# Kernel tuning notes

Hardware: AMD Instinct MI355X
Metric: run time of the kernel (lower is better)

Reference implementation:

```python
import jax, jax.numpy as jnp
import numpy as np

B, N, E = 2, 32768, 32768
DIM = 3
MP_STEPS = 2
H = 32  # hidden width; original bug: depth == hidden width (range(hidden))


def _ln(x, g, b):
    m = jnp.mean(x, axis=-1, keepdims=True)
    v = jnp.var(x, axis=-1, keepdims=True)
    return (x - m) * jax.lax.rsqrt(v + 1e-5) * g + b


def _mlp(x, Win, bin_, Wh, bh, Wout, bout, lng=None, lnb=None):
    # Linear -> ReLU -> [LN] -> H x (Linear -> ReLU -> [LN]) -> Linear -> ReLU
    h = jax.nn.relu(x @ Win + bin_)
    if lng is not None:
        h = _ln(h, lng[0], lnb[0])
        def body(h, p):
            W, b_, g_, bb = p
            return _ln(jax.nn.relu(h @ W + b_), g_, bb), None
        h, _ = jax.lax.scan(body, h, (Wh, bh, lng[1:], lnb[1:]))
    else:
        def body(h, p):
            W, b_ = p
            return jax.nn.relu(h @ W + b_), None
        h, _ = jax.lax.scan(body, h, (Wh, bh))
    return jax.nn.relu(h @ Wout + bout)


def _mk(key, din, h, dout, ln, pref):
    ks = jax.random.split(key, 3)
    d = {
        pref + 'Win': jax.random.normal(ks[0], (din, h), jnp.float32) / np.sqrt(din).astype(np.float32),
        pref + 'bin': jnp.zeros((h,), jnp.float32),
        pref + 'Wh': jax.random.normal(ks[1], (h, h, h), jnp.float32) / np.sqrt(h).astype(np.float32),
        pref + 'bh': jnp.zeros((h, h), jnp.float32),
        pref + 'Wout': jax.random.normal(ks[2], (h, dout), jnp.float32) / np.sqrt(h).astype(np.float32),
        pref + 'bout': jnp.zeros((dout,), jnp.float32),
    }
    if ln:
        d[pref + 'lng'] = jnp.ones((h + 1, h), jnp.float32)
        d[pref + 'lnb'] = jnp.zeros((h + 1, h), jnp.float32)
    return d


def setup_inputs() -> dict:
    key = jax.random.key(0)
    ks = jax.random.split(key, 10)
    inp = {
        'nodes': jax.random.normal(ks[0], (B, N, 6), jnp.float32),
        'edges': jax.random.normal(ks[1], (B, E, 1), jnp.float32),
        'gvec': jax.random.normal(ks[2], (B,), jnp.float32),
        'senders': jax.random.randint(ks[3], (B, E), 0, N, jnp.int32),
        'receivers': jax.random.randint(ks[4], (B, E), 0, N, jnp.int32),
    }
    inp.update(_mk(ks[5], 6 + 1, H, 16, False, 'ne_'))          # node encoder: node_dim+global
    inp.update(_mk(ks[6], 1 + DIM + 1, H, 16, False, 'ed_'))    # edge encoder: edge_dim+dim+1
    inp.update(_mk(ks[7], 16 + 2 * 16 + 1, H, 16, True, 'pe_')) # edge processor
    inp.update(_mk(ks[8], 16 + 16 + 1, H, 16, True, 'pv_'))     # node processor
    inp.update(_mk(ks[9], 16, H, DIM, False, 'de_'))            # decoder
    return inp


def reference(nodes, edges, gvec, senders, receivers,
              ne_Win, ne_bin, ne_Wh, ne_bh, ne_Wout, ne_bout,
              ed_Win, ed_bin, ed_Wh, ed_bh, ed_Wout, ed_bout,
              pe_Win, pe_bin, pe_Wh, pe_bh, pe_Wout, pe_bout, pe_lng, pe_lnb,
              pv_Win, pv_bin, pv_Wh, pv_bh, pv_Wout, pv_bout, pv_lng, pv_lnb,
              de_Win, de_bin, de_Wh, de_bh, de_Wout, de_bout):
    g_node = jnp.broadcast_to(gvec[:, None, None], (B, N, 1))  # global repeated per node
    g_edge = jnp.broadcast_to(gvec[:, None, None], (B, E, 1))  # global repeated per edge
    x = jnp.concatenate([nodes, g_node], axis=-1)  # [B,N,7]

    # relative edge features from sender/receiver positions (first DIM cols)
    pos = x[..., :DIM]
    si = senders[:, :, None]
    ri = receivers[:, :, None]
    rel = jnp.take_along_axis(pos, si, axis=1) - jnp.take_along_axis(pos, ri, axis=1)  # [B,E,3]
    nrm = jnp.linalg.norm(rel, axis=-1, keepdims=True)
    e_in = jnp.concatenate([edges, rel, nrm], axis=-1)  # [B,E,5]

    ve = _mlp(x, ne_Win, ne_bin, ne_Wh, ne_bh, ne_Wout, ne_bout)       # [B,N,16]
    ee = _mlp(e_in, ed_Win, ed_bin, ed_Wh, ed_bh, ed_Wout, ed_bout)    # [B,E,16]

    seg = jax.vmap(lambda e, r: jax.ops.segment_sum(e, r, num_segments=N))

    for _ in range(MP_STEPS):
        # phi_e: gather sender/receiver node states, concat, edge MLP
        vs = jnp.take_along_axis(ve, si, axis=1)  # [B,E,16]
        vr = jnp.take_along_axis(ve, ri, axis=1)
        ee = _mlp(jnp.concatenate([ee, vs, vr, g_edge], axis=-1),
                  pe_Win, pe_bin, pe_Wh, pe_bh, pe_Wout, pe_bout, pe_lng, pe_lnb)
        # phi_v: scatter-add edge states into receiver nodes, concat, node MLP
        agg = seg(ee, receivers)  # [B,N,16]
        ve = _mlp(jnp.concatenate([agg, ve, g_node], axis=-1),
                  pv_Win, pv_bin, pv_Wh, pv_bh, pv_Wout, pv_bout, pv_lng, pv_lnb)

    return _mlp(ve, de_Win, de_bin, de_Wh, de_bh, de_Wout, de_bout)  # [B,N,3]
```

## Files before the change

### kernel.cpp

```cpp
#include <hip/hip_runtime.h>

#define BB 2
#define NN 32768
#define EN 32768

typedef unsigned int u32;
typedef __attribute__((ext_vector_type(8)))  short bf16x8;
typedef __attribute__((ext_vector_type(2)))  float f32x2;
typedef __attribute__((ext_vector_type(16))) float f32x16;

union U4 { uint4 u; bf16x8 h; };

__device__ __forceinline__ u32 pk2(float lo, float hi) {
    u32 r;
    asm("v_cvt_pk_bf16_f32 %0, %1, %2" : "=v"(r) : "v"(lo), "v"(hi));
    return r;
}

__device__ __forceinline__ float xor32_sum(float x) {
    float y = x;
    asm("v_permlane32_swap_b32 %0, %1" : "+v"(x), "+v"(y));
    return x + y;
}

// ... 15 lines not shown
        f32x2 sv = ((p0+p1)+(p2+p3)) + ((p4+p5)+(p6+p7));
        f32x2 ta = __builtin_elementwise_fma(p0,p0,
                   __builtin_elementwise_fma(p1,p1,
                   __builtin_elementwise_fma(p2,p2, p3*p3)));
        f32x2 tb = __builtin_elementwise_fma(p4,p4,
                   __builtin_elementwise_fma(p5,p5,
                   __builtin_elementwise_fma(p6,p6, p7*p7)));
        f32x2 tv = ta + tb;
        float s = xor32_sum(sv.x + sv.y);
        float t = xor32_sum(tv.x + tv.y);
        float mu  = s * (1.f/32.f);
        float var = fmaf(-mu, mu, t * (1.f/32.f));
        float rs  = rsqrtf(var + 1e-5f);
        float nt  = -mu * rs;
        f32x2 rs2 = {rs, rs}, nt2 = {nt, nt};
        p0 = __builtin_elementwise_fma(p0, rs2, nt2);
        p1 = __builtin_elementwise_fma(p1, rs2, nt2);
        p2 = __builtin_elementwise_fma(p2, rs2, nt2);
        p3 = __builtin_elementwise_fma(p3, rs2, nt2);
        p4 = __builtin_elementwise_fma(p4, rs2, nt2);
        p5 = __builtin_elementwise_fma(p5, rs2, nt2);
        p6 = __builtin_elementwise_fma(p6, rs2, nt2);
        p7 = __builtin_elementwise_fma(p7, rs2, nt2);
    }
    U4 c;
    c.u.x = pk2(p0.x,p0.y); c.u.y = pk2(p1.x,p1.y);
    c.u.z = pk2(p2.x,p2.y); c.u.w = pk2(p3.x,p3.y);
    B0 = c.h;
    c.u.x = pk2(p4.x,p4.y); c.u.y = pk2(p5.x,p5.y);
    c.u.z = pk2(p6.x,p6.y); c.u.w = pk2(p7.x,p7.y);
    B1 = c.h;
}

__device__ __forceinline__ f32x16 load_biasC(const float* WB, int base, int h) {
    const float4* p = (const float4*)(WB + base + h*16);
    float4 a = p[0], b = p[1], c = p[2], d = p[3];
    f32x16 C = {a.x,a.y,a.z,a.w, b.x,b.y,b.z,b.w,
                c.x,c.y,c.z,c.w, d.x,d.y,d.z,d.w};
    return C;
}

template<int NT, bool LN>
__device__ __forceinline__ f32x16 mlp32(const bf16x8* bIn,
    const u32* WL, const float* WB, int lane, int h)
{
    constexpr int HB = NT*256;
    constexpr int BO = HB + 16384;
    U4 c;
    f32x16 D = load_biasC(WB, 0, h);
    #pragma unroll
    for (int t = 0; t < NT; ++t) {
        c.u = *(const uint4*)(WL + t*256 + lane*4);
        D = MF32(c.h, bIn[t], D);
    }
    c.u = *(const uint4*)(WL + HB + lane*4);        bf16x8 w0 = c.h;
    c.u = *(const uint4*)(WL + HB + 256 + lane*4);  bf16x8 w1 = c.h;
    c.u = *(const uint4*)(WL + HB + 512 + lane*4);  bf16x8 x0 = c.h;
    c.u = *(const uint4*)(WL + HB + 768 + lane*4);  bf16x8 x1 = c.h;
    f32x16 pb = load_biasC(WB, 32, h);
    bf16x8 B0, B1;
    transform32<LN>(D, B0, B1);
    #pragma unroll 4
    for (int l = 0; l < 32; ++l) {
        const int lp = (l+2 < 32) ? l+2 : 31;
        c.u = *(const uint4*)(WL + HB + lp*512 + lane*4);       bf16x8 nw0 = c.h;
        c.u = *(const uint4*)(WL + HB + lp*512 + 256 + lane*4); bf16x8 nw1 = c.h;
        const int lb_ = (l+1 < 32) ? l+1 : 31;
        f32x16 nb = load_biasC(WB, 32 + lb_*32, h);
        f32x16 E = MF32(w0, B0, pb);
        E = MF32(w1, B1, E);
        transform32<LN>(E, B0, B1);
        w0 = x0; w1 = x1; x0 = nw0; x1 = nw1; pb = nb;
    }
    c.u = *(const uint4*)(WL + BO + lane*4);        bf16x8 o0 = c.h;
    c.u = *(const uint4*)(WL + BO + 256 + lane*4);  bf16x8 o1 = c.h;
    f32x16 Co = load_biasC(WB, 1056, h);
    f32x16 O = MF32(o0, B0, Co);
    O = MF32(o1, B1, O);
    return O;
}

__device__ __forceinline__ void stage_weights32(
    u32* WL, float* WB, const u32* __restrict__ Wp,
    const float* __restrict__ bin, const float* __restrict__ bhid,
    const float* __restrict__ bo, int wtot, int nbo, int tid, int nthr)
{
    const int lane  = tid & 63;
    const int base0 = (tid >> 6) * 256;
    const int step  = (nthr >> 6) * 256;
    for (int C = base0; C < wtot; C += step)
        __builtin_amdgcn_global_load_lds(
            (const __attribute__((address_space(1))) u32*)(Wp + C + lane*4),
            (__attribute__((address_space(3))) u32*)(WL + C), 16, 0, 0);
    for (int i = tid; i < 1088; i += nthr) {
        float v;
        if (i < 32) {
            int w = i, hh = w>>4, r = w&15;
            int f = (r&3) + 8*(r>>2) + 4*hh;
            v = bin[f];
        } else if (i < 1056) {
            int l = (i-32)>>5, w = (i-32)&31, hh = w>>4, r = w&15;
            int f = (r&3) + 8*(r>>2) + 4*hh;
            v = bhid[l*32 + f];
        } else {
            int w = i-1056, hh = w>>4, r = w&15;
            int f = (r&3) + 8*(r>>2) + 4*hh;
            v = (f < nbo) ? bo[f] : 0.f;
        }
        WB[i] = v;
    }
    __syncthreads();
}

__device__ __forceinline__ void pack_body32(
    const float* __restrict__ Win, const float* __restrict__ Wh,
    const float* __restrict__ Wout, const float* __restrict__ lng,
    u32* __restrict__ dst, int din, int dout, int NT, int lb, int tid)
{
    int t = lb * 256 + tid;
    int binW = NT * 256;
    int tot = binW + 16384 + 512;
    if (t >= tot) return;
    float lo, hi;
    if (t < binW) {
        int tt = t>>8, rem = t&255, ln_ = rem>>2, d = rem&3;
        int hh = ln_>>5, m = ln_&31;
        int f0 = 16*tt + 4*hh + 2*(d&1) + 8*(d>>1);
        lo = (f0   < din) ? Win[f0*32 + m]     : 0.f;
        hi = (f0+1 < din) ? Win[(f0+1)*32 + m] : 0.f;
    } else if (t < binW + 16384) {
        int u = t - binW, l = u>>9, v = u&511;
        int tt = v>>8, rem = v&255, ln_ = rem>>2, d = rem&3;
        int hh = ln_>>5, m = ln_&31;
        int f0 = 16*tt + 4*hh + 2*(d&1) + 8*(d>>1);
        lo = Wh[l*1024 + f0*32 + m];
        hi = Wh[l*1024 + (f0+1)*32 + m];
        if (lng) { lo *= lng[l*32 + f0]; hi *= lng[l*32 + f0 + 1]; }
    } else {
        int u = t - binW - 16384;
        int tt = u>>8, rem = u&255, ln_ = rem>>2, d = rem&3;
        int hh = ln_>>5, m = ln_&31;
        int f0 = 16*tt + 4*hh + 2*(d&1) + 8*(d>>1);
        lo = (m < dout) ? Wout[f0*dout + m]     : 0.f;
        hi = (m < dout) ? Wout[(f0+1)*dout + m] : 0.f;
        if (lng) { lo *= lng[1024 + f0]; hi *= lng[1024 + f0 + 1]; }
    }
    dst[t] = pk2(lo, hi);
}

__device__ __forceinline__ void fold_body(
    const float* __restrict__ Wh,   const float* __restrict__ bh,
    const float* __restrict__ Wout, const float* __restrict__ bout,
    const float* __restrict__ lnb,  float* __restrict__ fb, int lb, int tid)
{
    int j = lb * 256 + tid;
    if (j < 1024) {
        int l = j >> 5, jj = j & 31;
        float acc = bh[j];
        #pragma unroll
        for (int k = 0; k < 32; ++k)
            acc = fmaf(lnb[l*32 + k], Wh[l*1024 + k*32 + jj], acc);
        fb[j] = acc;
    } else if (j < 1024 + 16) {
        int jj = j - 1024;
        float acc = bout[jj];
        #pragma unroll
        for (int k = 0; k < 32; ++k)
            acc = fmaf(lnb[1024 + k], Wout[k*16 + jj], acc);
        fb[j] = acc;
    }
}

__global__ __launch_bounds__(256) void prep_kernel(
    const float* ne_Win, const float* ne_Wh, const float* ne_Wout,
    const float* ed_Win, const float* ed_Wh, const float* ed_Wout,
    const float* pe_Win, const float* pe_Wh, const float* pe_Wout,
    const float* pe_lng, const float* pe_lnb, const float* pe_bh, const float* pe_bout,
    const float* pv_Win, const float* pv_Wh, const float* pv_Wout,
    const float* pv_lng, const float* pv_lnb, const float* pv_bh, const float* pv_bout,
    const float* de_Win, const float* de_Wh, const float* de_Wout,
    u32* Wne, u32* Wed, u32* Wpe, u32* Wpv, u32* Wde,
    float* Fpe, float* Fpv)
{
    int bx = blockIdx.x, tid = threadIdx.x;
    if      (bx < 67)  pack_body32(ne_Win, ne_Wh, ne_Wout, nullptr, Wne,  7, 16, 1, bx,       tid);
    else if (bx < 134) pack_body32(ed_Win, ed_Wh, ed_Wout, nullptr, Wed,  5, 16, 1, bx - 67,  tid);
    else if (bx < 204) pack_body32(pe_Win, pe_Wh, pe_Wout, pe_lng,  Wpe, 49, 16, 4, bx - 134, tid);
    else if (bx < 273) pack_body32(pv_Win, pv_Wh, pv_Wout, pv_lng,  Wpv, 33, 16, 3, bx - 204, tid);
    else if (bx < 340) pack_body32(de_Win, de_Wh, de_Wout, nullptr, Wde, 16,  3, 1, bx - 273, tid);
    else if (bx < 345) fold_body(pe_Wh, pe_bh, pe_Wout, pe_bout, pe_lnb, Fpe, bx - 340, tid);
    else               fold_body(pv_Wh, pv_bh, pv_Wout, pv_bout, pv_lnb, Fpv, bx - 345, tid);
}

__device__ __forceinline__ bf16x8 stage_chunk(const float* __restrict__ arr,
                                              size_t e, int h)
{
    const int off = h*4;
    float4 a = *(const float4*)(arr + e*16 + off);
    float4 b = *(const float4*)(arr + e*16 + off + 8);
    U4 c;
    c.u.x = pk2(a.x, a.y); c.u.y = pk2(a.z, a.w);
    c.u.z = pk2(b.x, b.y); c.u.w = pk2(b.z, b.w);
    return c.h;
}

#define WAVE_SETUP \
    const int lane = threadIdx.x & 63; \
    const int wid  = threadIdx.x >> 6; \
    const int el = lane & 31, h = lane >> 5;

__global__ __launch_bounds__(512, 4) void encode_kernel(
    const float* __restrict__ nodes, const float* __restrict__ edges,
    const float* __restrict__ gvec,
    const int* __restrict__ senders, const int* __restrict__ receivers,
    const u32* __restrict__ Wne, const float* __restrict__ ne_bin,
    const float* __restrict__ ne_bh, const float* __restrict__ ne_bout,
    const u32* __restrict__ Wed, const float* __restrict__ ed_bin,
    const float* __restrict__ ed_bh, const float* __restrict__ ed_bout,
    float* __restrict__ ve, float* __restrict__ ee)
{
    __shared__ __align__(16) u32 SL[17152 + 1088];
    u32* WL = SL;
    float* WB = (float*)(SL + 17152);
    WAVE_SETUP
    const bool edge_stage = blockIdx.x >= 256;
    stage_weights32(WL, WB,
                    edge_stage ? Wed : Wne,
                    edge_stage ? ed_bin : ne_bin,
                    edge_stage ? ed_bh : ne_bh,
                    edge_stage ? ed_bout : ne_bout,
                    17152, 16, threadIdx.x, 512);
    const int lb = edge_stage ? (blockIdx.x - 256) : blockIdx.x;
    const int e = (lb*8 + wid)*32 + el;
    const int b = e >> 15;
    bf16x8 a0;
    {
        uint4 w; w.x = 0u; w.y = 0u; w.z = 0u; w.w = 0u;
        if (!edge_stage) {
            if (h == 0) {
                float2 v01 = *(const float2*)(nodes + (size_t)e*6);
                float2 v23 = *(const float2*)(nodes + (size_t)e*6 + 2);
                w.x = pk2(v01.x, v01.y); w.y = pk2(v23.x, v23.y);
            } else {
                float2 v45 = *(const float2*)(nodes + (size_t)e*6 + 4);
                w.x = pk2(v45.x, v45.y); w.y = pk2(gvec[b], 0.f);
            }
        } else {
            int s = senders[e], r = receivers[e];
            const float* ps = nodes + ((size_t)b*NN + s)*6;
            const float* pr = nodes + ((size_t)b*NN + r)*6;
            float2 s01 = *(const float2*)ps; float s2v = ps[2];
            float2 r01 = *(const float2*)pr; float r2v = pr[2];
            float r0 = s01.x - r01.x, r1 = s01.y - r01.y, r2 = s2v - r2v;
            if (h == 0) {
                w.x = pk2(edges[e], r0); w.y = pk2(r1, r2);
            } else {
                w.x = pk2(sqrtf(r0*r0 + r1*r1 + r2*r2), 0.f);
            }
        }
        U4 c; c.u = w; a0 = c.h;
    }
    float* dst = edge_stage ? ee : ve;
    f32x16 O = mlp32<1, false>(&a0, WL, WB, lane, h);
    float4 s1, s2;
    s1.x = fmaxf(O[0], 0.f); s1.y = fmaxf(O[1], 0.f);
    s1.z = fmaxf(O[2], 0.f); s1.w = fmaxf(O[3], 0.f);
    s2.x = fmaxf(O[4], 0.f); s2.y = fmaxf(O[5], 0.f);
    s2.z = fmaxf(O[6], 0.f); s2.w = fmaxf(O[7], 0.f);
    *(float4*)(dst + (size_t)e*16 + h*4)     = s1;
    *(float4*)(dst + (size_t)e*16 + h*4 + 8) = s2;
}

__global__ __launch_bounds__(512, 2) void edge_update_kernel(
    const float* __restrict__ gvec,
    const int* __restrict__ senders, const int* __restrict__ receivers,
    const float* __restrict__ ve, float* __restrict__ ee, float* __restrict__ agg,
    const u32* __restrict__ Wp, const float* __restrict__ bin,
    const float* __restrict__ fb)
{
    __shared__ __align__(16) u32 SL[17920 + 1088 + 8*544];
    u32* WL = SL;
    float* WB = (float*)(SL + 17920);
    WAVE_SETUP
    float* X = (float*)(SL + 19008) + wid*544;
    stage_weights32(WL, WB, Wp, bin, fb, fb + 1024, 17920, 16, threadIdx.x, 512);
    const int e0 = (blockIdx.x*8 + wid)*32;
    const int e  = e0 + el;
    const int b  = e >> 15;
    const int s  = senders[e], r_ = receivers[e];
    bf16x8 a[4];
    a[0] = stage_chunk(ee, (size_t)e, h);
    a[1] = stage_chunk(ve, (size_t)b*NN + s, h);
    a[2] = stage_chunk(ve, (size_t)b*NN + r_, h);
    {
        uint4 w; w.x = (h == 0) ? pk2(gvec[b], 0.f) : 0u;
        w.y = 0u; w.z = 0u; w.w = 0u;
        U4 c; c.u = w; a[3] = c.h;
    }
    f32x16 O = mlp32<4, true>(a, WL, WB, lane, h);
    float4 s1, s2;
    s1.x = fmaxf(O[0], 0.f); s1.y = fmaxf(O[1], 0.f);
    s1.z = fmaxf(O[2], 0.f); s1.w = fmaxf(O[3], 0.f);
    s2.x = fmaxf(O[4], 0.f); s2.y = fmaxf(O[5], 0.f);
    s2.z = fmaxf(O[6], 0.f); s2.w = fmaxf(O[7], 0.f);
    *(float4*)(ee + (size_t)e*16 + h*4)     = s1;
    *(float4*)(ee + (size_t)e*16 + h*4 + 8) = s2;
    *(float4*)(X + el*17 + h*4)     = s1;
    *(float4*)(X + el*17 + h*4 + 8) = s2;
    const int feat = lane & 15;
    #pragma unroll
    for (int rr = 0; rr < 8; ++rr) {
        int m = (lane >> 4)*8 + rr;
        float v = X[m*17 + feat];
        int rc = __shfl(r_, m);
        int eg = e0 + m;
        atomicAdd(agg + ((size_t)(eg >> 15)*NN + rc)*16 + feat, v);
    }
}

template<bool DEC>
__global__ __launch_bounds__(512, 2) void node_update_kernel(
    const float* __restrict__ gvec,
    const float* __restrict__ agg, float* __restrict__ ve,
    const u32* __restrict__ Wp, const float* __restrict__ bin,
    const float* __restrict__ fb,
    const u32* __restrict__ Wde, const float* __restrict__ de_bin,
    const float* __restrict__ de_bh, const float* __restrict__ de_bout,
    float* __restrict__ out)
{
    __shared__ __align__(16) u32 SL[DEC ? (18752 + 17152 + 1088) : 18752];
    u32* WL = SL;
    float* WB = (float*)(SL + 17664);
    u32* WL2 = SL + 18752;
    float* WB2 = (float*)(SL + 18752 + 17152);
    WAVE_SETUP
    stage_weights32(WL, WB, Wp, bin, fb, fb + 1024, 17664, 16, threadIdx.x, 512);
    if (DEC)
        stage_weights32(WL2, WB2, Wde, de_bin, de_bh, de_bout, 17152, 3, threadIdx.x, 512);
    const int e = (blockIdx.x*8 + wid)*32 + el;
    const int b = e >> 15;
    bf16x8 a[3];
    a[0] = stage_chunk(agg, (size_t)e, h);
    a[1] = stage_chunk(ve,  (size_t)e, h);
    {
        uint4 w; w.x = (h == 0) ? pk2(gvec[b], 0.f) : 0u;
        w.y = 0u; w.z = 0u; w.w = 0u;
        U4 c; c.u = w; a[2] = c.h;
    }
    f32x16 O = mlp32<3, true>(a, WL, WB, lane, h);
    if (!DEC) {
        float4 s1, s2;
        s1.x = fmaxf(O[0], 0.f); s1.y = fmaxf(O[1], 0.f);
        s1.z = fmaxf(O[2], 0.f); s1.w = fmaxf(O[3], 0.f);
        s2.x = fmaxf(O[4], 0.f); s2.y = fmaxf(O[5], 0.f);
        s2.z = fmaxf(O[6], 0.f); s2.w = fmaxf(O[7], 0.f);
        *(float4*)(ve + (size_t)e*16 + h*4)     = s1;
        *(float4*)(ve + (size_t)e*16 + h*4 + 8) = s2;
    } else {
        bf16x8 D0, D1;
        transform32<false>(O, D0, D1);
        f32x16 O2 = mlp32<1, false>(&D0, WL2, WB2, lane, h);
        if (h == 0) {
            out[(size_t)e*3 + 0] = fmaxf(O2[0], 0.f);
            out[(size_t)e*3 + 1] = fmaxf(O2[1], 0.f);
            out[(size_t)e*3 + 2] = fmaxf(O2[2], 0.f);
        }
    }
}

extern "C" void kernel_launch(void* const* d_in, const int* in_sizes, int n_in,
                              void* d_out, int out_size, void* d_ws, size_t ws_size,
                              hipStream_t stream)
{
    const float* nodes     = (const float*)d_in[0];
    const float* edges     = (const float*)d_in[1];
    const float* gvec      = (const float*)d_in[2];
    const int*   senders   = (const int*)  d_in[3];
    const int*   receivers = (const int*)  d_in[4];

    const float* ne_Win  = (const float*)d_in[5];
    const float* ne_bin  = (const float*)d_in[6];
    const float* ne_Wh   = (const float*)d_in[7];
    const float* ne_bh   = (const float*)d_in[8];
    const float* ne_Wout = (const float*)d_in[9];
    const float* ne_bout = (const float*)d_in[10];

    const float* ed_Win  = (const float*)d_in[11];
    const float* ed_bin  = (const float*)d_in[12];
    const float* ed_Wh   = (const float*)d_in[13];
    const float* ed_bh   = (const float*)d_in[14];
    const float* ed_Wout = (const float*)d_in[15];
    const float* ed_bout = (const float*)d_in[16];

    const float* pe_Win  = (const float*)d_in[17];
    const float* pe_bin  = (const float*)d_in[18];
    const float* pe_Wh   = (const float*)d_in[19];
    const float* pe_bh   = (const float*)d_in[20];
    const float* pe_Wout = (const float*)d_in[21];
    const float* pe_bout = (const float*)d_in[22];
    const float* pe_lng  = (const float*)d_in[23];
    const float* pe_lnb  = (const float*)d_in[24];

    const float* pv_Win  = (const float*)d_in[25];
    const float* pv_bin  = (const float*)d_in[26];
    const float* pv_Wh   = (const float*)d_in[27];
    const float* pv_bh   = (const float*)d_in[28];
    const float* pv_Wout = (const float*)d_in[29];
    const float* pv_bout = (const float*)d_in[30];
    const float* pv_lng  = (const float*)d_in[31];
    const float* pv_lnb  = (const float*)d_in[32];

    const float* de_Win  = (const float*)d_in[33];
    const float* de_bin  = (const float*)d_in[34];
    const float* de_Wh   = (const float*)d_in[35];
    const float* de_bh   = (const float*)d_in[36];
    const float* de_Wout = (const float*)d_in[37];
    const float* de_bout = (const float*)d_in[38];

    float* ve   = (float*)d_ws;
    float* ee   = ve   + (size_t)1048576;
    float* agg0 = ee   + (size_t)1048576;
    float* agg1 = agg0 + (size_t)1048576;
    u32* Wne = (u32*)(agg1 + (size_t)1048576);
    u32* Wed = Wne + 17152;
    u32* Wpe = Wed + 17152;
    u32* Wpv = Wpe + 17920;
    u32* Wde = Wpv + 17664;
    float* Fpe = (float*)(Wde + 17152);
    float* Fpv = Fpe + 1040;

    prep_kernel<<<350, dim3(256), 0, stream>>>(
        ne_Win, ne_Wh, ne_Wout,
        ed_Win, ed_Wh, ed_Wout,
        pe_Win, pe_Wh, pe_Wout, pe_lng, pe_lnb, pe_bh, pe_bout,
        pv_Win, pv_Wh, pv_Wout, pv_lng, pv_lnb, pv_bh, pv_bout,
        de_Win, de_Wh, de_Wout,
        Wne, Wed, Wpe, Wpv, Wde, Fpe, Fpv);

    hipMemsetAsync(agg0, 0, (size_t)2 * 1048576 * sizeof(float), stream);

    encode_kernel<<<512, dim3(512), 0, stream>>>(nodes, edges, gvec, senders, receivers,
        Wne, ne_bin, ne_bh, ne_bout,
        Wed, ed_bin, ed_bh, ed_bout, ve, ee);

    edge_update_kernel<<<256, dim3(512), 0, stream>>>(gvec, senders, receivers,
        ve, ee, agg0, Wpe, pe_bin, Fpe);
    node_update_kernel<false><<<256, dim3(512), 0, stream>>>(gvec, agg0, ve,
        Wpv, pv_bin, Fpv, Wde, de_bin, de_bh, de_bout, (float*)d_out);
    edge_update_kernel<<<256, dim3(512), 0, stream>>>(gvec, senders, receivers,
        ve, ee, agg1, Wpe, pe_bin, Fpe);
    node_update_kernel<true><<<256, dim3(512), 0, stream>>>(gvec, agg1, ve,
        Wpv, pv_bin, Fpv, Wde, de_bin, de_bh, de_bout, (float*)d_out);
}
```

Before: 241.6 us.

## Fold LayerNorm mean subtraction into post-matmul affine correction for LN MLPs

Adds an mlp32_ln path in which each hidden layer multiplies the un-normalized ReLU output (bf16) by the gamma-folded weights. The LayerNorm is applied afterwards as rs*E + (-mu*rs)*rho + beta, where rho = column sums of the gamma-scaled weights, precomputed in prep_kernel. The intent is to take the per-layer normalize pass off the critical path before the next MFMA, so the statistics run in parallel with the matmul. The cost is a larger bias table in LDS (rho/beta per layer), extra prep blocks, and precision risk because raw activations are quantized to bf16 before normalization.

```diff
diff --git a/kernel.cpp b/kernel.cpp
--- a/kernel.cpp
+++ b/kernel.cpp
@@ -71,12 +71,28 @@
     B1 = c.h;
 }
 
+__device__ __forceinline__ void stats8(
+    f32x2 p0, f32x2 p1, f32x2 p2, f32x2 p3,
+    f32x2 p4, f32x2 p5, f32x2 p6, f32x2 p7, float& rs, float& q)
+{
+    f32x2 sv = ((p0+p1)+(p2+p3)) + ((p4+p5)+(p6+p7));
+    f32x2 ta = __builtin_elementwise_fma(p0,p0,
+               __builtin_elementwise_fma(p1,p1,
+               __builtin_elementwise_fma(p2,p2, p3*p3)));
+    f32x2 tb = __builtin_elementwise_fma(p4,p4,
+               __builtin_elementwise_fma(p5,p5,
+               __builtin_elementwise_fma(p6,p6, p7*p7)));
+    f32x2 tv = ta + tb;
+    float s = xor32_sum(sv.x + sv.y);
+    float t = xor32_sum(tv.x + tv.y);
+    float mu  = s * (1.f/32.f);
+    float var = fmaf(-mu, mu, t * (1.f/32.f));
+    rs = rsqrtf(var + 1e-5f);
+    q  = -mu * rs;
+}
+
 __device__ __forceinline__ f32x16 load_biasC(const float* WB, int base, int h) {
-    const float4* p = (const float4*)(WB + base + h*16);
-    float4 a = p[0], b = p[1], c = p[2], d = p[3];
-    f32x16 C = {a.x,a.y,a.z,a.w, b.x,b.y,b.z,b.w,
-                c.x,c.y,c.z,c.w, d.x,d.y,d.z,d.w};
-    return C;
+    return *(const f32x16*)(WB + base + h*16);
 }
 
 template<int NT, bool LN>
@@ -119,18 +135,131 @@
     return O;
 }
 
-__device__ __forceinline__ void stage_weights32(
-    u32* WL, float* WB, const u32* __restrict__ Wp,
-    const float* __restrict__ bin, const float* __restrict__ bhid,
-    const float* __restrict__ bo, int wtot, int nbo, int tid, int nthr)
-{
-    const int lane  = tid & 63;
-    const int base0 = (tid >> 6) * 256;
-    const int step  = (nthr >> 6) * 256;
-    for (int C = base0; C < wtot; C += step)
+#define LN_POST(E1, E2) \
+    { \
+        f32x2 q2 = {q, q}, rs2 = {rs, rs}; \
+        f32x2 b0 = {bet[0],bet[1]}, b1 = {bet[2],bet[3]}, b2 = {bet[4],bet[5]}, b3 = {bet[6],bet[7]}; \
+        f32x2 b4 = {bet[8],bet[9]}, b5 = {bet[10],bet[11]}, b6 = {bet[12],bet[13]}, b7 = {bet[14],bet[15]}; \
+        f32x2 r0 = {rho[0],rho[1]}, r1 = {rho[2],rho[3]}, r2 = {rho[4],rho[5]}, r3 = {rho[6],rho[7]}; \
+        f32x2 r4 = {rho[8],rho[9]}, r5 = {rho[10],rho[11]}, r6 = {rho[12],rho[13]}, r7 = {rho[14],rho[15]}; \
+        f32x2 c0 = __builtin_elementwise_fma(q2, r0, b0); \
+        f32x2 c1 = __builtin_elementwise_fma(q2, r1, b1); \
+        f32x2 c2 = __builtin_elementwise_fma(q2, r2, b2); \
+        f32x2 c3 = __builtin_elementwise_fma(q2, r3, b3); \
+        f32x2 c4 = __builtin_elementwise_fma(q2, r4, b4); \
+        f32x2 c5 = __builtin_elementwise_fma(q2, r5, b5); \
+        f32x2 c6 = __builtin_elementwise_fma(q2, r6, b6); \
+        f32x2 c7 = __builtin_elementwise_fma(q2, r7, b7); \
+        f32x2 e; \
+        e = (f32x2){E1[0],E1[1]};   c0 = __builtin_elementwise_fma(rs2, e, c0); \
+        e = (f32x2){E1[2],E1[3]};   c1 = __builtin_elementwise_fma(rs2, e, c1); \
+        e = (f32x2){E1[4],E1[5]};   c2 = __builtin_elementwise_fma(rs2, e, c2); \
+        e = (f32x2){E1[6],E1[7]};   c3 = __builtin_elementwise_fma(rs2, e, c3); \
+        e = (f32x2){E1[8],E1[9]};   c4 = __builtin_elementwise_fma(rs2, e, c4); \
+        e = (f32x2){E1[10],E1[11]}; c5 = __builtin_elementwise_fma(rs2, e, c5); \
+        e = (f32x2){E1[12],E1[13]}; c6 = __builtin_elementwise_fma(rs2, e, c6); \
+        e = (f32x2){E1[14],E1[15]}; c7 = __builtin_elementwise_fma(rs2, e, c7); \
+        e = (f32x2){E2[0],E2[1]};   p0 = __builtin_elementwise_fma(rs2, e, c0); \
+        e = (f32x2){E2[2],E2[3]};   p1 = __builtin_elementwise_fma(rs2, e, c1); \
+        e = (f32x2){E2[4],E2[5]};   p2 = __builtin_elementwise_fma(rs2, e, c2); \
+        e = (f32x2){E2[6],E2[7]};   p3 = __builtin_elementwise_fma(rs2, e, c3); \
+        e = (f32x2){E2[8],E2[9]};   p4 = __builtin_elementwise_fma(rs2, e, c4); \
+        e = (f32x2){E2[10],E2[11]}; p5 = __builtin_elementwise_fma(rs2, e, c5); \
+        e = (f32x2){E2[12],E2[13]}; p6 = __builtin_elementwise_fma(rs2, e, c6); \
+        e = (f32x2){E2[14],E2[15]}; p7 = __builtin_elementwise_fma(rs2, e, c7); \
+    }
+
+template<int NT>
+__device__ __forceinline__ f32x16 mlp32_ln(const bf16x8* bIn,
+    const u32* WL, const float* WB, int lane, int h)
+{
+    constexpr int HB = NT*256;
+    constexpr int BO = HB + 16384;
+    U4 c;
+    f32x16 Z;
+    #pragma unroll
+    for (int i = 0; i < 16; ++i) Z[i] = 0.f;
+    f32x16 D = load_biasC(WB, 0, h);
+    #pragma unroll
+    for (int t = 0; t < NT; ++t) {
+        c.u = *(const uint4*)(WL + t*256 + lane*4);
+        D = MF32(c.h, bIn[t], D);
+    }
+    const f32x2 zz = {0.f, 0.f};
+    f32x2 p0 = {D[0],D[1]},  p1 = {D[2],D[3]},  p2 = {D[4],D[5]},  p3 = {D[6],D[7]};
+    f32x2 p4 = {D[8],D[9]},  p5 = {D[10],D[11]},p6 = {D[12],D[13]},p7 = {D[14],D[15]};
+    p0 = __builtin_elementwise_max(p0, zz); p1 = __builtin_elementwise_max(p1, zz);
+    p2 = __builtin_elementwise_max(p2, zz); p3 = __builtin_elementwise_max(p3, zz);
+    p4 = __builtin_elementwise_max(p4, zz); p5 = __builtin_elementwise_max(p5, zz);
+    p6 = __builtin_elementwise_max(p6, zz); p7 = __builtin_elementwise_max(p7, zz);
+    float rs, q;
+    stats8(p0,p1,p2,p3,p4,p5,p6,p7, rs, q);
+    bf16x8 H0, H1;
+    {
+        U4 cc;
+        cc.u.x = pk2(p0.x,p0.y); cc.u.y = pk2(p1.x,p1.y);
+        cc.u.z = pk2(p2.x,p2.y); cc.u.w = pk2(p3.x,p3.y); H0 = cc.h;
+        cc.u.x = pk2(p4.x,p4.y); cc.u.y = pk2(p5.x,p5.y);
+        cc.u.z = pk2(p6.x,p6.y); cc.u.w = pk2(p7.x,p7.y); H1 = cc.h;
+    }
+    c.u = *(const uint4*)(WL + HB + lane*4);        bf16x8 w0 = c.h;
+    c.u = *(const uint4*)(WL + HB + 256 + lane*4);  bf16x8 w1 = c.h;
+    c.u = *(const uint4*)(WL + HB + 512 + lane*4);  bf16x8 x0 = c.h;
+    c.u = *(const uint4*)(WL + HB + 768 + lane*4);  bf16x8 x1 = c.h;
+    f32x16 bet = load_biasC(WB, 32, h);
+    f32x16 rho = load_biasC(WB, 64, h);
+    #pragma unroll 2
+    for (int l = 0; l < 32; ++l) {
+        f32x16 E1 = MF32(w0, H0, Z);
+        f32x16 E2 = MF32(w1, H1, Z);
+        const int lp = (l+2 < 32) ? l+2 : 31;
+        c.u = *(const uint4*)(WL + HB + lp*512 + lane*4);       bf16x8 nw0 = c.h;
+        c.u = *(const uint4*)(WL + HB + lp*512 + 256 + lane*4); bf16x8 nw1 = c.h;
+        const int lb_ = (l+1 < 32) ? l+1 : 31;
+        f32x16 betN = load_biasC(WB, 32 + lb_*64, h);
+        f32x16 rhoN = load_biasC(WB, 64 + lb_*64, h);
+        LN_POST(E1, E2)
+        p0 = __builtin_elementwise_max(p0, zz); p1 = __builtin_elementwise_max(p1, zz);
+        p2 = __builtin_elementwise_max(p2, zz); p3 = __builtin_elementwise_max(p3, zz);
+        p4 = __builtin_elementwise_max(p4, zz); p5 = __builtin_elementwise_max(p5, zz);
+        p6 = __builtin_elementwise_max(p6, zz); p7 = __builtin_elementwise_max(p7, zz);
+        stats8(p0,p1,p2,p3,p4,p5,p6,p7, rs, q);
+        {
+            U4 cc;
+            cc.u.x = pk2(p0.x,p0.y); cc.u.y = pk2(p1.x,p1.y);
+            cc.u.z = pk2(p2.x,p2.y); cc.u.w = pk2(p3.x,p3.y); H0 = cc.h;
+            cc.u.x = pk2(p4.x,p4.y); cc.u.y = pk2(p5.x,p5.y);
+            cc.u.z = pk2(p6.x,p6.y); cc.u.w = pk2(p7.x,p7.y); H1 = cc.h;
+        }
+        w0 = x0; w1 = x1; x0 = nw0; x1 = nw1; bet = betN; rho = rhoN;
+    }
+    c.u = *(const uint4*)(WL + BO + lane*4);        bf16x8 o0 = c.h;
+    c.u = *(const uint4*)(WL + BO + 256 + lane*4);  bf16x8 o1 = c.h;
+    bet = load_biasC(WB, 2080, h);
+    rho = load_biasC(WB, 2112, h);
+    f32x16 E1 = MF32(o0, H0, Z);
+    f32x16 E2 = MF32(o1, H1, Z);
+    LN_POST(E1, E2)
+    f32x16 O = {p0.x,p0.y, p1.x,p1.y, p2.x,p2.y, p3.x,p3.y,
+                p4.x,p4.y, p5.x,p5.y, p6.x,p6.y, p7.x,p7.y};
+    return O;
+}
+
+__device__ __forceinline__ void stage_dma(u32* WL, const u32* __restrict__ Wp,
+                                          int wtot, int tid, int nthr)
+{
+    const int lane = tid & 63;
+    const int step = (nthr >> 6) * 256;
+    for (int C = (tid >> 6)*256; C < wtot; C += step)
         __builtin_amdgcn_global_load_lds(
             (const __attribute__((address_space(1))) u32*)(Wp + C + lane*4),
             (__attribute__((address_space(3))) u32*)(WL + C), 16, 0, 0);
+}
+
+__device__ __forceinline__ void stage_bias(float* WB,
+    const float* __restrict__ bin, const float* __restrict__ bhid,
+    const float* __restrict__ bo, int nbo, int tid, int nthr)
+{
     for (int i = tid; i < 1088; i += nthr) {
         float v;
         if (i < 32) {
@@ -148,6 +277,46 @@
         }
         WB[i] = v;
     }
+}
+
+__device__ __forceinline__ void stage_bias_ln(float* WB,
+    const float* __restrict__ bin, const float* __restrict__ F,
+    int tid, int nthr)
+{
+    for (int i = tid; i < 2144; i += nthr) {
+        float v;
+        if (i < 32) {
+            int hh = i>>4, r = i&15;
+            int f = (r&3) + 8*(r>>2) + 4*hh;
+            v = bin[f];
+        } else {
+            int u = i - 32, l = u>>6, w = u&63, sel = w>>5, ww = w&31;
+            int hh = ww>>4, r = ww&15;
+            int f = (r&3) + 8*(r>>2) + 4*hh;
+            if (l < 32) v = sel ? F[1040 + l*32 + f] : F[l*32 + f];
+            else        v = (f < 16) ? (sel ? F[2064 + f] : F[1024 + f]) : 0.f;
+        }
+        WB[i] = v;
+    }
+}
+
+__device__ __forceinline__ void stage_weights32(
+    u32* WL, float* WB, const u32* __restrict__ Wp,
+    const float* __restrict__ bin, const float* __restrict__ bhid,
+    const float* __restrict__ bo, int wtot, int nbo, int tid, int nthr)
+{
+    stage_dma(WL, Wp, wtot, tid, nthr);
+    stage_bias(WB, bin, bhid, bo, nbo, tid, nthr);
+    __syncthreads();
+}
+
+__device__ __forceinline__ void stage_weights32_ln(
+    u32* WL, float* WB, const u32* __restrict__ Wp,
+    const float* __restrict__ bin, const float* __restrict__ F,
+    int wtot, int tid, int nthr)
+{
+    stage_dma(WL, Wp, wtot, tid, nthr);
+    stage_bias_ln(WB, bin, F, tid, nthr);
     __syncthreads();
 }
 
@@ -190,23 +359,23 @@
 __device__ __forceinline__ void fold_body(
     const float* __restrict__ Wh,   const float* __restrict__ bh,
     const float* __restrict__ Wout, const float* __restrict__ bout,
-    const float* __restrict__ lnb,  float* __restrict__ fb, int lb, int tid)
+    const float* __restrict__ vec,  float* __restrict__ dst, int lb, int tid)
 {
     int j = lb * 256 + tid;
     if (j < 1024) {
         int l = j >> 5, jj = j & 31;
-        float acc = bh[j];
+        float acc = bh ? bh[j] : 0.f;
         #pragma unroll
         for (int k = 0; k < 32; ++k)
-            acc = fmaf(lnb[l*32 + k], Wh[l*1024 + k*32 + jj], acc);
-        fb[j] = acc;
+            acc = fmaf(vec[l*32 + k], Wh[l*1024 + k*32 + jj], acc);
+        dst[j] = acc;
     } else if (j < 1024 + 16) {
         int jj = j - 1024;
-        float acc = bout[jj];
+        float acc = bout ? bout[jj] : 0.f;
         #pragma unroll
         for (int k = 0; k < 32; ++k)
-            acc = fmaf(lnb[1024 + k], Wout[k*16 + jj], acc);
-        fb[j] = acc;
+            acc = fmaf(vec[1024 + k], Wout[k*16 + jj], acc);
+        dst[j] = acc;
     }
 }
 
@@ -227,8 +396,10 @@
     else if (bx < 204) pack_body32(pe_Win, pe_Wh, pe_Wout, pe_lng,  Wpe, 49, 16, 4, bx - 134, tid);
     else if (bx < 273) pack_body32(pv_Win, pv_Wh, pv_Wout, pv_lng,  Wpv, 33, 16, 3, bx - 204, tid);
     else if (bx < 340) pack_body32(de_Win, de_Wh, de_Wout, nullptr, Wde, 16,  3, 1, bx - 273, tid);
-    else if (bx < 345) fold_body(pe_Wh, pe_bh, pe_Wout, pe_bout, pe_lnb, Fpe, bx - 340, tid);
-    else               fold_body(pv_Wh, pv_bh, pv_Wout, pv_bout, pv_lnb, Fpv, bx - 345, tid);
+    else if (bx < 345) fold_body(pe_Wh, pe_bh, pe_Wout, pe_bout, pe_lnb, Fpe,        bx - 340, tid);
+    else if (bx < 350) fold_body(pe_Wh, nullptr, pe_Wout, nullptr, pe_lng, Fpe+1040, bx - 345, tid);
+    else if (bx < 355) fold_body(pv_Wh, pv_bh, pv_Wout, pv_bout, pv_lnb, Fpv,        bx - 350, tid);
+    else               fold_body(pv_Wh, nullptr, pv_Wout, nullptr, pv_lng, Fpv+1040, bx - 355, tid);
 }
 
 __device__ __forceinline__ bf16x8 stage_chunk(const float* __restrict__ arr,
@@ -241,6 +412,18 @@
     c.u.x = pk2(a.x, a.y); c.u.y = pk2(a.z, a.w);
     c.u.z = pk2(b.x, b.y); c.u.w = pk2(b.z, b.w);
     return c.h;
+}
+
+__device__ __forceinline__ void store_relu(float* __restrict__ dst, size_t e,
+                                           int h, f32x16 O)
+{
+    float4 s1, s2;
+    s1.x = fmaxf(O[0], 0.f); s1.y = fmaxf(O[1], 0.f);
+    s1.z = fmaxf(O[2], 0.f); s1.w = fmaxf(O[3], 0.f);
+    s2.x = fmaxf(O[4], 0.f); s2.y = fmaxf(O[5], 0.f);
+    s2.z = fmaxf(O[6], 0.f); s2.w = fmaxf(O[7], 0.f);
+    *(float4*)(dst + e*16 + h*4)     = s1;
+    *(float4*)(dst + e*16 + h*4 + 8) = s2;
 }
 
 #define WAVE_SETUP \
@@ -258,7 +441,7 @@
     const float* __restrict__ ed_bh, const float* __restrict__ ed_bout,
     float* __restrict__ ve, float* __restrict__ ee)
 {
-    __shared__ __align__(16) u32 SL[17152 + 1088];
+    __shared__ __align__(64) u32 SL[17152 + 1088];
     u32* WL = SL;
     float* WB = (float*)(SL + 17152);
     WAVE_SETUP
@@ -301,13 +484,7 @@
     }
     float* dst = edge_stage ? ee : ve;
     f32x16 O = mlp32<1, false>(&a0, WL, WB, lane, h);
-    float4 s1, s2;
-    s1.x = fmaxf(O[0], 0.f); s1.y = fmaxf(O[1], 0.f);
-    s1.z = fmaxf(O[2], 0.f); s1.w = fmaxf(O[3], 0.f);
-    s2.x = fmaxf(O[4], 0.f); s2.y = fmaxf(O[5], 0.f);
-    s2.z = fmaxf(O[6], 0.f); s2.w = fmaxf(O[7], 0.f);
-    *(float4*)(dst + (size_t)e*16 + h*4)     = s1;
-    *(float4*)(dst + (size_t)e*16 + h*4 + 8) = s2;
+    store_relu(dst, (size_t)e, h, O);
 }
 
 __global__ __launch_bounds__(512, 2) void edge_update_kernel(
@@ -315,14 +492,14 @@
     const int* __restrict__ senders, const int* __restrict__ receivers,
     const float* __restrict__ ve, float* __restrict__ ee, float* __restrict__ agg,
     const u32* __restrict__ Wp, const float* __restrict__ bin,
-    const float* __restrict__ fb)
-{
-    __shared__ __align__(16) u32 SL[17920 + 1088 + 8*544];
+    const float* __restrict__ F)
+{
+    __shared__ __align__(64) u32 SL[17920 + 2144 + 8*544];
     u32* WL = SL;
     float* WB = (float*)(SL + 17920);
     WAVE_SETUP
-    float* X = (float*)(SL + 19008) + wid*544;
-    stage_weights32(WL, WB, Wp, bin, fb, fb + 1024, 17920, 16, threadIdx.x, 512);
+    float* X = (float*)(SL + 20064) + wid*544;
+    stage_weights32_ln(WL, WB, Wp, bin, F, 17920, threadIdx.x, 512);
     const int e0 = (blockIdx.x*8 + wid)*32;
     const int e  = e0 + el;
     const int b  = e >> 15;
@@ -336,7 +513,7 @@
         w.y = 0u; w.z = 0u; w.w = 0u;
         U4 c; c.u = w; a[3] = c.h;
     }
-    f32x16 O = mlp32<4, true>(a, WL, WB, lane, h);
+    f32x16 O = mlp32_ln<4>(a, WL, WB, lane, h);
     float4 s1, s2;
     s1.x = fmaxf(O[0], 0.f); s1.y = fmaxf(O[1], 0.f);
     s1.z = fmaxf(O[2], 0.f); s1.w = fmaxf(O[3], 0.f);
@@ -362,20 +539,21 @@
     const float* __restrict__ gvec,
     const float* __restrict__ agg, float* __restrict__ ve,
     const u32* __restrict__ Wp, const float* __restrict__ bin,
-    const float* __restrict__ fb,
+    const float* __restrict__ F,
     const u32* __restrict__ Wde, const float* __restrict__ de_bin,
     const float* __restrict__ de_bh, const float* __restrict__ de_bout,
     float* __restrict__ out)
 {
-    __shared__ __align__(16) u32 SL[DEC ? (18752 + 17152 + 1088) : 18752];
+    __shared__ __align__(64) u32 SL[DEC ? (19808 + 17152 + 1088) : 19808];
     u32* WL = SL;
     float* WB = (float*)(SL + 17664);
-    u32* WL2 = SL + 18752;
-    float* WB2 = (float*)(SL + 18752 + 17152);
+    u32* WL2 = SL + 19808;
+    float* WB2 = (float*)(SL + 19808 + 17152);
     WAVE_SETUP
-    stage_weights32(WL, WB, Wp, bin, fb, fb + 1024, 17664, 16, threadIdx.x, 512);
+    stage_weights32_ln(WL, WB, Wp, bin, F, 17664, threadIdx.x, 512);
     if (DEC)
-        stage_weights32(WL2, WB2, Wde, de_bin, de_bh, de_bout, 17152, 3, threadIdx.x, 512);
+        stage_weights32(WL2, WB2, Wde, de_bin, de_bh, de_bout, 17152, 3,
+                        threadIdx.x, 512);
     const int e = (blockIdx.x*8 + wid)*32 + el;
     const int b = e >> 15;
     bf16x8 a[3];
@@ -386,15 +564,9 @@
         w.y = 0u; w.z = 0u; w.w = 0u;
         U4 c; c.u = w; a[2] = c.h;
     }
-    f32x16 O = mlp32<3, true>(a, WL, WB, lane, h);
+    f32x16 O = mlp32_ln<3>(a, WL, WB, lane, h);
     if (!DEC) {
-        float4 s1, s2;
-        s1.x = fmaxf(O[0], 0.f); s1.y = fmaxf(O[1], 0.f);
-        s1.z = fmaxf(O[2], 0.f); s1.w = fmaxf(O[3], 0.f);
-        s2.x = fmaxf(O[4], 0.f); s2.y = fmaxf(O[5], 0.f);
-        s2.z = fmaxf(O[6], 0.f); s2.w = fmaxf(O[7], 0.f);
-        *(float4*)(ve + (size_t)e*16 + h*4)     = s1;
-        *(float4*)(ve + (size_t)e*16 + h*4 + 8) = s2;
+        store_relu(ve, (size_t)e, h, O);
     } else {
         bf16x8 D0, D1;
         transform32<false>(O, D0, D1);
@@ -466,9 +638,9 @@
     u32* Wpv = Wpe + 17920;
     u32* Wde = Wpv + 17664;
     float* Fpe = (float*)(Wde + 17152);
-    float* Fpv = Fpe + 1040;
-
-    prep_kernel<<<350, dim3(256), 0, stream>>>(
+    float* Fpv = Fpe + 2080;
+
+    prep_kernel<<<360, dim3(256), 0, stream>>>(
         ne_Win, ne_Wh, ne_Wout,
         ed_Win, ed_Wh, ed_Wout,
         pe_Win, pe_Wh, pe_Wout, pe_lng, pe_lnb, pe_bh, pe_bout,
```

New measurement: 244.1 us. No clear change (+1.1%).

## Store node/edge states as bf16 and fold global feature into per-batch input bias

Applied to the files above, without the earlier changes.

Intermediate node and edge states are now stored as packed bf16 instead of fp32, which halves gather/store traffic in the edge and node update kernels and removes the per-load fp32-to-bf16 conversion. The global-vector input column is folded into a per-batch input bias computed in prep_kernel, so the first-layer K tiles drop from 4 to 3 (edge) and from 3 to 2 (node). Blocks pick the bias by batch index, and the bias load becomes a single vector load. This adds bf16 rounding of the stored states and relies on the block-to-batch mapping (blockIdx & 128).

```diff
diff --git a/kernel.cpp b/kernel.cpp
--- a/kernel.cpp
+++ b/kernel.cpp
@@ -72,11 +72,7 @@
 }
 
 __device__ __forceinline__ f32x16 load_biasC(const float* WB, int base, int h) {
-    const float4* p = (const float4*)(WB + base + h*16);
-    float4 a = p[0], b = p[1], c = p[2], d = p[3];
-    f32x16 C = {a.x,a.y,a.z,a.w, b.x,b.y,b.z,b.w,
-                c.x,c.y,c.z,c.w, d.x,d.y,d.z,d.w};
-    return C;
+    return *(const f32x16*)(WB + base + h*16);
 }
 
 template<int NT, bool LN>
@@ -119,18 +115,21 @@
     return O;
 }
 
-__device__ __forceinline__ void stage_weights32(
-    u32* WL, float* WB, const u32* __restrict__ Wp,
-    const float* __restrict__ bin, const float* __restrict__ bhid,
-    const float* __restrict__ bo, int wtot, int nbo, int tid, int nthr)
-{
-    const int lane  = tid & 63;
-    const int base0 = (tid >> 6) * 256;
-    const int step  = (nthr >> 6) * 256;
-    for (int C = base0; C < wtot; C += step)
+__device__ __forceinline__ void stage_dma(u32* WL, const u32* __restrict__ Wp,
+                                          int wtot, int tid, int nthr)
+{
+    const int lane = tid & 63;
+    const int step = (nthr >> 6) * 256;
+    for (int C = (tid >> 6)*256; C < wtot; C += step)
         __builtin_amdgcn_global_load_lds(
             (const __attribute__((address_space(1))) u32*)(Wp + C + lane*4),
             (__attribute__((address_space(3))) u32*)(WL + C), 16, 0, 0);
+}
+
+__device__ __forceinline__ void stage_bias(float* WB,
+    const float* __restrict__ bin, const float* __restrict__ bhid,
+    const float* __restrict__ bo, int nbo, int tid, int nthr)
+{
     for (int i = tid; i < 1088; i += nthr) {
         float v;
         if (i < 32) {
@@ -148,6 +147,15 @@
         }
         WB[i] = v;
     }
+}
+
+__device__ __forceinline__ void stage_weights32(
+    u32* WL, float* WB, const u32* __restrict__ Wp,
+    const float* __restrict__ bin, const float* __restrict__ bhid,
+    const float* __restrict__ bo, int wtot, int nbo, int tid, int nthr)
+{
+    stage_dma(WL, Wp, wtot, tid, nthr);
+    stage_bias(WB, bin, bhid, bo, nbo, tid, nthr);
     __syncthreads();
 }
 
@@ -215,20 +223,32 @@
     const float* ed_Win, const float* ed_Wh, const float* ed_Wout,
     const float* pe_Win, const float* pe_Wh, const float* pe_Wout,
     const float* pe_lng, const float* pe_lnb, const float* pe_bh, const float* pe_bout,
+    const float* pe_bin,
     const float* pv_Win, const float* pv_Wh, const float* pv_Wout,
     const float* pv_lng, const float* pv_lnb, const float* pv_bh, const float* pv_bout,
+    const float* pv_bin,
     const float* de_Win, const float* de_Wh, const float* de_Wout,
+    const float* gvec,
     u32* Wne, u32* Wed, u32* Wpe, u32* Wpv, u32* Wde,
     float* Fpe, float* Fpv)
 {
     int bx = blockIdx.x, tid = threadIdx.x;
     if      (bx < 67)  pack_body32(ne_Win, ne_Wh, ne_Wout, nullptr, Wne,  7, 16, 1, bx,       tid);
     else if (bx < 134) pack_body32(ed_Win, ed_Wh, ed_Wout, nullptr, Wed,  5, 16, 1, bx - 67,  tid);
-    else if (bx < 204) pack_body32(pe_Win, pe_Wh, pe_Wout, pe_lng,  Wpe, 49, 16, 4, bx - 134, tid);
-    else if (bx < 273) pack_body32(pv_Win, pv_Wh, pv_Wout, pv_lng,  Wpv, 33, 16, 3, bx - 204, tid);
-    else if (bx < 340) pack_body32(de_Win, de_Wh, de_Wout, nullptr, Wde, 16,  3, 1, bx - 273, tid);
-    else if (bx < 345) fold_body(pe_Wh, pe_bh, pe_Wout, pe_bout, pe_lnb, Fpe, bx - 340, tid);
-    else               fold_body(pv_Wh, pv_bh, pv_Wout, pv_bout, pv_lnb, Fpv, bx - 345, tid);
+    else if (bx < 203) pack_body32(pe_Win, pe_Wh, pe_Wout, pe_lng,  Wpe, 48, 16, 3, bx - 134, tid);
+    else if (bx < 271) pack_body32(pv_Win, pv_Wh, pv_Wout, pv_lng,  Wpv, 32, 16, 2, bx - 203, tid);
+    else if (bx < 338) pack_body32(de_Win, de_Wh, de_Wout, nullptr, Wde, 16,  3, 1, bx - 271, tid);
+    else if (bx < 343) fold_body(pe_Wh, pe_bh, pe_Wout, pe_bout, pe_lnb, Fpe, bx - 338, tid);
+    else if (bx < 348) fold_body(pv_Wh, pv_bh, pv_Wout, pv_bout, pv_lnb, Fpv, bx - 343, tid);
+    else {
+        if (tid < 64) {
+            int b = tid >> 5, f = tid & 31;
+            Fpe[1040 + tid] = pe_bin[f] + gvec[b] * pe_Win[48*32 + f];
+        } else if (tid < 128) {
+            int u = tid - 64, b = u >> 5, f = u & 31;
+            Fpv[1040 + u] = pv_bin[f] + gvec[b] * pv_Win[32*32 + f];
+        }
+    }
 }
 
 __device__ __forceinline__ bf16x8 stage_chunk(const float* __restrict__ arr,
@@ -256,9 +276,9 @@
     const float* __restrict__ ne_bh, const float* __restrict__ ne_bout,
     const u32* __restrict__ Wed, const float* __restrict__ ed_bin,
     const float* __restrict__ ed_bh, const float* __restrict__ ed_bout,
-    float* __restrict__ ve, float* __restrict__ ee)
-{
-    __shared__ __align__(16) u32 SL[17152 + 1088];
+    u32* __restrict__ veB, u32* __restrict__ eeB)
+{
+    __shared__ __align__(64) u32 SL[17152 + 1088];
     u32* WL = SL;
     float* WB = (float*)(SL + 17152);
     WAVE_SETUP
@@ -299,51 +319,47 @@
         }
         U4 c; c.u = w; a0 = c.h;
     }
-    float* dst = edge_stage ? ee : ve;
+    u32* dstB = edge_stage ? eeB : veB;
     f32x16 O = mlp32<1, false>(&a0, WL, WB, lane, h);
+    U4 cc;
+    cc.u.x = pk2(fmaxf(O[0],0.f), fmaxf(O[1],0.f));
+    cc.u.y = pk2(fmaxf(O[2],0.f), fmaxf(O[3],0.f));
+    cc.u.z = pk2(fmaxf(O[4],0.f), fmaxf(O[5],0.f));
+    cc.u.w = pk2(fmaxf(O[6],0.f), fmaxf(O[7],0.f));
+    *(uint4*)(dstB + (size_t)e*8 + h*4) = cc.u;
+}
+
+__global__ __launch_bounds__(512, 2) void edge_update_kernel(
+    const int* __restrict__ senders, const int* __restrict__ receivers,
+    const u32* __restrict__ veB, u32* __restrict__ eeB, float* __restrict__ agg,
+    const u32* __restrict__ Wp, const float* __restrict__ F)
+{
+    __shared__ __align__(64) u32 SL[17664 + 1088 + 8*544];
+    u32* WL = SL;
+    float* WB = (float*)(SL + 17664);
+    WAVE_SETUP
+    float* X = (float*)(SL + 18752) + wid*544;
+    const float* binSel = F + 1040 + ((blockIdx.x & 128) ? 32 : 0);
+    stage_weights32(WL, WB, Wp, binSel, F, F + 1024, 17664, 16, threadIdx.x, 512);
+    const int e0 = (blockIdx.x*8 + wid)*32;
+    const int e  = e0 + el;
+    const int b  = e >> 15;
+    const int s  = senders[e], r_ = receivers[e];
+    bf16x8 a[3];
+    U4 c;
+    c.u = *(const uint4*)(eeB + (size_t)e*8 + h*4);               a[0] = c.h;
+    c.u = *(const uint4*)(veB + ((size_t)b*NN + s )*8 + h*4);     a[1] = c.h;
+    c.u = *(const uint4*)(veB + ((size_t)b*NN + r_)*8 + h*4);     a[2] = c.h;
+    f32x16 O = mlp32<3, true>(a, WL, WB, lane, h);
     float4 s1, s2;
     s1.x = fmaxf(O[0], 0.f); s1.y = fmaxf(O[1], 0.f);
     s1.z = fmaxf(O[2], 0.f); s1.w = fmaxf(O[3], 0.f);
     s2.x = fmaxf(O[4], 0.f); s2.y = fmaxf(O[5], 0.f);
     s2.z = fmaxf(O[6], 0.f); s2.w = fmaxf(O[7], 0.f);
-    *(float4*)(dst + (size_t)e*16 + h*4)     = s1;
-    *(float4*)(dst + (size_t)e*16 + h*4 + 8) = s2;
-}
-
-__global__ __launch_bounds__(512, 2) void edge_update_kernel(
-    const float* __restrict__ gvec,
-    const int* __restrict__ senders, const int* __restrict__ receivers,
-    const float* __restrict__ ve, float* __restrict__ ee, float* __restrict__ agg,
-    const u32* __restrict__ Wp, const float* __restrict__ bin,
-    const float* __restrict__ fb)
-{
-    __shared__ __align__(16) u32 SL[17920 + 1088 + 8*544];
-    u32* WL = SL;
-    float* WB = (float*)(SL + 17920);
-    WAVE_SETUP
-    float* X = (float*)(SL + 19008) + wid*544;
-    stage_weights32(WL, WB, Wp, bin, fb, fb + 1024, 17920, 16, threadIdx.x, 512);
-    const int e0 = (blockIdx.x*8 + wid)*32;
-    const int e  = e0 + el;
-    const int b  = e >> 15;
-    const int s  = senders[e], r_ = receivers[e];
-    bf16x8 a[4];
-    a[0] = stage_chunk(ee, (size_t)e, h);
-    a[1] = stage_chunk(ve, (size_t)b*NN + s, h);
-    a[2] = stage_chunk(ve, (size_t)b*NN + r_, h);
-    {
-        uint4 w; w.x = (h == 0) ? pk2(gvec[b], 0.f) : 0u;
-        w.y = 0u; w.z = 0u; w.w = 0u;
-        U4 c; c.u = w; a[3] = c.h;
-    }
-    f32x16 O = mlp32<4, true>(a, WL, WB, lane, h);
-    float4 s1, s2;
-    s1.x = fmaxf(O[0], 0.f); s1.y = fmaxf(O[1], 0.f);
-    s1.z = fmaxf(O[2], 0.f); s1.w = fmaxf(O[3], 0.f);
-    s2.x = fmaxf(O[4], 0.f); s2.y = fmaxf(O[5], 0.f);
-    s2.z = fmaxf(O[6], 0.f); s2.w = fmaxf(O[7], 0.f);
-    *(float4*)(ee + (size_t)e*16 + h*4)     = s1;
-    *(float4*)(ee + (size_t)e*16 + h*4 + 8) = s2;
+    U4 cc;
+    cc.u.x = pk2(s1.x, s1.y); cc.u.y = pk2(s1.z, s1.w);
+    cc.u.z = pk2(s2.x, s2.y); cc.u.w = pk2(s2.z, s2.w);
+    *(uint4*)(eeB + (size_t)e*8 + h*4) = cc.u;
     *(float4*)(X + el*17 + h*4)     = s1;
     *(float4*)(X + el*17 + h*4 + 8) = s2;
     const int feat = lane & 15;
@@ -359,42 +375,40 @@
 
 template<bool DEC>
 __global__ __launch_bounds__(512, 2) void node_update_kernel(
-    const float* __restrict__ gvec,
-    const float* __restrict__ agg, float* __restrict__ ve,
-    const u32* __restrict__ Wp, const float* __restrict__ bin,
-    const float* __restrict__ fb,
+    const float* __restrict__ agg, u32* __restrict__ veB,
+    const u32* __restrict__ Wp, const float* __restrict__ F,
     const u32* __restrict__ Wde, const float* __restrict__ de_bin,
     const float* __restrict__ de_bh, const float* __restrict__ de_bout,
     float* __restrict__ out)
 {
-    __shared__ __align__(16) u32 SL[DEC ? (18752 + 17152 + 1088) : 18752];
+    __shared__ __align__(64) u32 SL[DEC ? (17408 + 17152 + 1088 + 1088) : (17408 + 1088)];
     u32* WL = SL;
-    float* WB = (float*)(SL + 17664);
-    u32* WL2 = SL + 18752;
-    float* WB2 = (float*)(SL + 18752 + 17152);
+    u32* WL2 = SL + 17408;
+    float* WB  = (float*)(SL + (DEC ? 34560 : 17408));
+    float* WB2 = (float*)(SL + 35648);
     WAVE_SETUP
-    stage_weights32(WL, WB, Wp, bin, fb, fb + 1024, 17664, 16, threadIdx.x, 512);
+    const float* binSel = F + 1040 + ((blockIdx.x & 128) ? 32 : 0);
+    stage_weights32(WL, WB, Wp, binSel, F, F + 1024, 17408, 16, threadIdx.x, 512);
     if (DEC)
-        stage_weights32(WL2, WB2, Wde, de_bin, de_bh, de_bout, 17152, 3, threadIdx.x, 512);
+        stage_weights32(WL2, WB2, Wde, de_bin, de_bh, de_bout, 17152, 3,
+                        threadIdx.x, 512);
     const int e = (blockIdx.x*8 + wid)*32 + el;
     const int b = e >> 15;
-    bf16x8 a[3];
+    bf16x8 a[2];
     a[0] = stage_chunk(agg, (size_t)e, h);
-    a[1] = stage_chunk(ve,  (size_t)e, h);
     {
-        uint4 w; w.x = (h == 0) ? pk2(gvec[b], 0.f) : 0u;
-        w.y = 0u; w.z = 0u; w.w = 0u;
-        U4 c; c.u = w; a[2] = c.h;
-    }
-    f32x16 O = mlp32<3, true>(a, WL, WB, lane, h);
+        U4 c;
+        c.u = *(const uint4*)(veB + (size_t)e*8 + h*4);
+        a[1] = c.h;
+    }
+    f32x16 O = mlp32<2, true>(a, WL, WB, lane, h);
     if (!DEC) {
-        float4 s1, s2;
-        s1.x = fmaxf(O[0], 0.f); s1.y = fmaxf(O[1], 0.f);
-        s1.z = fmaxf(O[2], 0.f); s1.w = fmaxf(O[3], 0.f);
-        s2.x = fmaxf(O[4], 0.f); s2.y = fmaxf(O[5], 0.f);
-        s2.z = fmaxf(O[6], 0.f); s2.w = fmaxf(O[7], 0.f);
-        *(float4*)(ve + (size_t)e*16 + h*4)     = s1;
-        *(float4*)(ve + (size_t)e*16 + h*4 + 8) = s2;
+        U4 cc;
+        cc.u.x = pk2(fmaxf(O[0],0.f), fmaxf(O[1],0.f));
+        cc.u.y = pk2(fmaxf(O[2],0.f), fmaxf(O[3],0.f));
+        cc.u.z = pk2(fmaxf(O[4],0.f), fmaxf(O[5],0.f));
+        cc.u.w = pk2(fmaxf(O[6],0.f), fmaxf(O[7],0.f));
+        *(uint4*)(veB + (size_t)e*8 + h*4) = cc.u;
     } else {
         bf16x8 D0, D1;
         transform32<false>(O, D0, D1);
@@ -460,34 +474,36 @@
     float* ee   = ve   + (size_t)1048576;
     float* agg0 = ee   + (size_t)1048576;
     float* agg1 = agg0 + (size_t)1048576;
+    u32* veB = (u32*)ve;
+    u32* eeB = (u32*)ee;
     u32* Wne = (u32*)(agg1 + (size_t)1048576);
     u32* Wed = Wne + 17152;
     u32* Wpe = Wed + 17152;
-    u32* Wpv = Wpe + 17920;
-    u32* Wde = Wpv + 17664;
+    u32* Wpv = Wpe + 17664;
+    u32* Wde = Wpv + 17408;
     float* Fpe = (float*)(Wde + 17152);
-    float* Fpv = Fpe + 1040;
-
-    prep_kernel<<<350, dim3(256), 0, stream>>>(
+    float* Fpv = Fpe + 1104;
+
+    prep_kernel<<<349, dim3(256), 0, stream>>>(
         ne_Win, ne_Wh, ne_Wout,
         ed_Win, ed_Wh, ed_Wout,
-        pe_Win, pe_Wh, pe_Wout, pe_lng, pe_lnb, pe_bh, pe_bout,
-        pv_Win, pv_Wh, pv_Wout, pv_lng, pv_lnb, pv_bh, pv_bout,
-        de_Win, de_Wh, de_Wout,
+        pe_Win, pe_Wh, pe_Wout, pe_lng, pe_lnb, pe_bh, pe_bout, pe_bin,
+        pv_Win, pv_Wh, pv_Wout, pv_lng, pv_lnb, pv_bh, pv_bout, pv_bin,
+        de_Win, de_Wh, de_Wout, gvec,
         Wne, Wed, Wpe, Wpv, Wde, Fpe, Fpv);
 
     hipMemsetAsync(agg0, 0, (size_t)2 * 1048576 * sizeof(float), stream);
 
     encode_kernel<<<512, dim3(512), 0, stream>>>(nodes, edges, gvec, senders, receivers,
         Wne, ne_bin, ne_bh, ne_bout,
-        Wed, ed_bin, ed_bh, ed_bout, ve, ee);
-
-    edge_update_kernel<<<256, dim3(512), 0, stream>>>(gvec, senders, receivers,
-        ve, ee, agg0, Wpe, pe_bin, Fpe);
-    node_update_kernel<false><<<256, dim3(512), 0, stream>>>(gvec, agg0, ve,
-        Wpv, pv_bin, Fpv, Wde, de_bin, de_bh, de_bout, (float*)d_out);
-    edge_update_kernel<<<256, dim3(512), 0, stream>>>(gvec, senders, receivers,
-        ve, ee, agg1, Wpe, pe_bin, Fpe);
-    node_update_kernel<true><<<256, dim3(512), 0, stream>>>(gvec, agg1, ve,
-        Wpv, pv_bin, Fpv, Wde, de_bin, de_bh, de_bout, (float*)d_out);
-}
+        Wed, ed_bin, ed_bh, ed_bout, veB, eeB);
+
+    edge_update_kernel<<<256, dim3(512), 0, stream>>>(senders, receivers,
+        veB, eeB, agg0, Wpe, Fpe);
+    node_update_kernel<false><<<256, dim3(512), 0, stream>>>(agg0, veB,
+        Wpv, Fpv, Wde, de_bin, de_bh, de_bout, (float*)d_out);
+    edge_update_kernel<<<256, dim3(512), 0, stream>>>(senders, receivers,
+        veB, eeB, agg1, Wpe, Fpe);
+    node_update_kernel<true><<<256, dim3(512), 0, stream>>>(agg1, veB,
+        Wpv, Fpv, Wde, de_bin, de_bh, de_bout, (float*)d_out);
+}
```

Measured after the change: 237.5 us. Within noise of the previous version (-1.7%).
